# Kernel optimization log

Measured on AMD Instinct MI355X. Metric: run time of the kernel, lower is better.

## Reference

```python
import jax, jax.numpy as jnp
import numpy as np
from jax import lax
from jax.scipy.ndimage import map_coordinates

L = 10  # unrolled iterations (LayerNo)


def _conv(x, w, b):
    # x [N,C,H,W], w [O,I,3,3] -> 'SAME' padding == padding=1 for k=3
    y = lax.conv_general_dilated(x, w, (1, 1), 'SAME',
                                 dimension_numbers=('NCHW', 'OIHW', 'NCHW'))
    return y + b[None, :, None, None]


def _prelu(x, a):
    return jnp.where(x >= 0, x, a * x)


def _block(x, w1, b1, a1, w2, b2, a2, w3, b3):
    x = _prelu(_conv(x, w1, b1), a1)
    x = _prelu(_conv(x, w2, b2), a2)
    return _conv(x, w3, b3)


def _radon_forward(img, theta, det_count):
    # img [S,S]; parallel-beam line integrals -> [A, det_count]
    S = img.shape[0]
    c = (S - 1) / 2.0
    s = jnp.arange(det_count, dtype=img.dtype) - (det_count - 1) / 2.0
    t = jnp.arange(S, dtype=img.dtype) - (S - 1) / 2.0

    def one(a):
        ca, sa = jnp.cos(a), jnp.sin(a)
        x = s[:, None] * ca - t[None, :] * sa  # [D,S] sample cols
        y = s[:, None] * sa + t[None, :] * ca  # [D,S] sample rows
        vals = map_coordinates(img, [y + c, x + c], order=1, mode='constant', cval=0.0)
        return vals.sum(axis=1)

    return jax.vmap(one)(theta)


def _radon_backprojection(sino, theta, S):
    # sino [A,D] -> [S,S] (adjoint smear with bilinear detector interpolation)
    A, D = sino.shape
    c = (S - 1) / 2.0
    dc = (D - 1) / 2.0
    ax = jnp.arange(S, dtype=sino.dtype) - c
    Y, X = jnp.meshgrid(ax, ax, indexing='ij')  # row=y, col=x

    def one(row, a):
        ca, sa = jnp.cos(a), jnp.sin(a)
        sidx = (X * ca + Y * sa + dc).ravel()
        return map_coordinates(row, [sidx], order=1, mode='constant', cval=0.0).reshape(S, S)

    return jax.vmap(one)(sino, theta).sum(axis=0)


def _filter_sinogram(sino):
    # Ram-Lak ramp filter along detector axis with FBP normalization pi/(2*A)
    A, D = sino.shape
    n = 2048  # next power of two >= 2*D (D=729)
    F = jnp.fft.rfft(sino, n=n, axis=-1)
    ramp = (2.0 * jnp.fft.rfftfreq(n)).astype(sino.dtype)
    out = jnp.fft.irfft(F * ramp, n=n, axis=-1)[..., :D]
    return out * (jnp.pi / (2.0 * A))


def _forward(cond, x0, g, theta, theta_label,
             dw1, db1, da1, dw2, db2, da2, dw3, db3,
             pw1, pb1, pa1, pw2, pb2, pa2, pw3, pb3):
    S = x0.shape[2]
    A, D = g.shape[2], g.shape[3]
    h = jnp.zeros((1, 5, A, D), dtype=g.dtype)
    f = jnp.zeros((1, 5, S, S), dtype=g.dtype)
    for i in range(L):
        Op_f = _radon_forward(f[0, 1], theta, D)[None, None]          # [1,1,A,D]
        h = h + _block(jnp.concatenate([h, Op_f, g], axis=1),
                       dw1[i], db1[i], da1[i], dw2[i], db2[i], da2[i], dw3[i], db3[i])
        h1 = _filter_sinogram(h[0, 0])                                 # [A,D]
        OpAdj_h = _radon_backprojection(h1, theta, S)[None, None]      # [1,1,S,S]
        f = f + _block(jnp.concatenate([f, OpAdj_h], axis=1),
                       pw1[i], pb1[i], pa1[i], pw2[i], pb2[i], pa2[i], pw3[i], pb3[i])
    return (f[:, 0:1], f[:, 0:1], f[:, 0:1])


def setup_inputs() -> dict:
    key = jax.random.key(0)
    ks = jax.random.split(key, 12)
    S, A, D = 512, 60, 729

    def xavier(k, shp):
        cout, cin = shp[1], shp[2]
        std = np.sqrt(2.0 / ((cin + cout) * 9.0)).astype(np.float32)
        return jax.random.normal(k, shp, dtype=jnp.float32) * std

    ang = jnp.linspace(0.0, np.pi, A, endpoint=False).astype(jnp.float32)
    return {
        'cond': jax.random.normal(ks[0], (1, 1, S, S), dtype=jnp.float32),
        'x0': jax.random.normal(ks[1], (1, 1, S, S), dtype=jnp.float32),
        'g': jax.random.normal(ks[2], (1, 1, A, D), dtype=jnp.float32),
        'theta': ang,
        'theta_label': ang,
        'dw1': xavier(ks[3], (L, 32, 7, 3, 3)), 'db1': jnp.zeros((L, 32), jnp.float32), 'da1': 0.25 * jnp.ones((L,), jnp.float32),
        'dw2': xavier(ks[4], (L, 32, 32, 3, 3)), 'db2': jnp.zeros((L, 32), jnp.float32), 'da2': 0.25 * jnp.ones((L,), jnp.float32),
        'dw3': xavier(ks[5], (L, 5, 32, 3, 3)), 'db3': jnp.zeros((L, 5), jnp.float32),
        'pw1': xavier(ks[6], (L, 32, 6, 3, 3)), 'pb1': jnp.zeros((L, 32), jnp.float32), 'pa1': 0.25 * jnp.ones((L,), jnp.float32),
        'pw2': xavier(ks[7], (L, 32, 32, 3, 3)), 'pb2': jnp.zeros((L, 32), jnp.float32), 'pa2': 0.25 * jnp.ones((L,), jnp.float32),
        'pw3': xavier(ks[8], (L, 5, 32, 3, 3)), 'pb3': jnp.zeros((L, 5), jnp.float32),
    }


def reference(cond, x0, g, theta, theta_label,
              dw1, db1, da1, dw2, db2, da2, dw3, db3,
              pw1, pb1, pa1, pw2, pb2, pa2, pw3, pb3):
    return _forward(cond, x0, g, theta, theta_label,
                    dw1, db1, da1, dw2, db2, da2, dw3, db3,
                    pw1, pb1, pa1, pw2, pb2, pa2, pw3, pb3)
```

## Files before the change

### kernel.cpp

```cpp
#include <hip/hip_runtime.h>
#include <math.h>

#define SS 512
#define AANG 60
#define DDET 729
#define NPIX (SS*SS)
#define NSIN (AANG*DDET)
#define NTAPS 1457
#define DRS 768

typedef float v4u __attribute__((ext_vector_type(4), aligned(4)));
typedef float v4a __attribute__((ext_vector_type(4), aligned(16)));
typedef float v2u __attribute__((ext_vector_type(2), aligned(8)));
typedef float v2a __attribute__((ext_vector_type(2), aligned(4)));
typedef short short8 __attribute__((ext_vector_type(8)));
typedef float f32x4 __attribute__((ext_vector_type(4)));

__device__ inline unsigned short f2bf(float x){
  unsigned u = __float_as_uint(x);
  return (unsigned short)((u + 0x7fffu + ((u >> 16) & 1u)) >> 16);
}

__global__ void trig_kernel(const float* __restrict__ theta, float* __restrict__ trig){
  int a = threadIdx.x;
  if (a < AANG){ trig[a] = cosf(theta[a]); trig[AANG+a] = sinf(theta[a]); }
}

__global__ void taps_kernel(float* __restrict__ taps){
  __shared__ double red[256];
  int m  = blockIdx.x;
  int mm = m - 728;
  double s = 0.0;
  for (int k = 1 + (int)threadIdx.x; k <= 1023; k += 256){
    int phase = (k*mm) & 2047;
    s += (double)k * cos((double)phase * (M_PI/1024.0));
  }
  red[threadIdx.x] = s;
  __syncthreads();
  for (int off=128; off; off>>=1){
    if ((int)threadIdx.x < off) red[threadIdx.x] += red[threadIdx.x+off];
    __syncthreads();
  }
  if (threadIdx.x==0){
    double x = (red[0]*(1.0/512.0) + ((mm & 1) ? -1.0 : 1.0)) / 2048.0;
    taps[m] = (float)(x * (M_PI/120.0));
  }
}

__global__ void transpose_all(const float* __restrict__ s2, float* __restrict__ d2,
                              const float* __restrict__ s5, float* __restrict__ d5){
  int idx = blockIdx.x*256 + (int)threadIdx.x;
  const float* src; float* dst;
  int Cout = 5, Cin = 32;
  if      (idx < 14400){              src=s2; dst=d2; }
  else if (idx < 28800){ idx-=14400;  src=s5; dst=d5; }
  else return;
  int t = idx % 9; int r = idx/9;
  int i = r % Cin; r /= Cin;
  int o = r % Cout; int l = r/Cout;
  dst[((l*Cin+i)*9+t)*Cout+o] = src[idx];
}

__global__ void transpose_w8(const float* __restrict__ src, float* __restrict__ dst, int Cin){
  int idx = blockIdx.x*256 + (int)threadIdx.x;
  int tot = 10*32*Cin*9;
  if (idx >= tot) return;
  int t = idx % 9; int r = idx/9;
  int i = r % Cin; r /= Cin;
  int o = r % 32; int l = r/32;
  int cg = o >> 3, u = o & 7;
  dst[(((l*Cin + i)*4 + cg)*9 + t)*8 + u] = src[idx];
}

__global__ void prep_bimg(const float* __restrict__ w, unsigned short* __restrict__ B){
  int idx = blockIdx.x*256 + (int)threadIdx.x;
  if (idx >= 10*9*2*64*8) return;
  int j    =  idx        & 7;
  int lane = (idx >> 3)  & 63;
  int n    = (idx >> 9)  & 1;
  int r    =  idx >> 10;
  int tap = r % 9, l = r / 9;
  int c = (lane >> 4)*8 + j;
  int o = n*16 + (lane & 15);
  float x = w[(((size_t)(l*32+o)*32 + c)*9) + tap];
  unsigned short hb = f2bf(x);
  float hf = __uint_as_float((unsigned)hb << 16);
  unsigned short lb = f2bf(x - hf);
  size_t d = (size_t)l*18432 + (size_t)tap*2048 + n*1024 + lane*8 + j;
  B[d]       = hb;
  B[d + 512] = lb;
}

__global__ void prep_bimg3(const float* __restrict__ w, unsigned short* __restrict__ B){
  int idx = blockIdx.x*256 + (int)threadIdx.x;
  if (idx >= 10*9*64*8) return;
  int j    =  idx       & 7;
  int lane = (idx >> 3) & 63;
  int r    =  idx >> 9;
  int tap = r % 9, l = r / 9;
  int c = (lane >> 4)*8 + j;
  int o = lane & 15;
  float x = (o < 5) ? w[(((size_t)(l*5+o)*32 + c)*9) + tap] : 0.f;
  unsigned short hb = f2bf(x);
  float hf = __uint_as_float((unsigned)hb << 16);
  unsigned short lb = f2bf(x - hf);
  size_t d = (size_t)l*9216 + (size_t)tap*1024 + lane*8 + j;
  B[d]       = hb;
  B[d + 512] = lb;
}

__device__ inline void clipr(float al, float ial, float be, float lo, float hi,
                             float& A, float& B, bool& empty){
  if (fabsf(al) < 1e-7f){ if (be < lo || be > hi) empty = true; return; }
  float t0 = (lo - be)*ial, t1 = (hi - be)*ial;
  float mn = fminf(t0,t1), mx = fmaxf(t0,t1);
  A = fmaxf(A, mn); B = fminf(B, mx);
}

__device__ inline float samp_guard(const float* __restrict__ base, float aR, float bR,
                                   float aC, float bC, int t){
  float tp = (float)t - 255.5f;
  float R = fmaf(aR, tp, bR);
  float C = fmaf(aC, tp, bC);
  float rf = floorf(R), cf = floorf(C);
  int r0 = (int)rf, c0 = (int)cf;
  int r1 = r0+1,    c1 = c0+1;
  float fr = R - rf, fc = C - cf;
  bool r0ok = (r0>=0 && r0<SS), r1ok = (r1>=0 && r1<SS);
  bool c0ok = (c0>=0 && c0<SS), c1ok = (c1>=0 && c1<SS);
  float v00 = (r0ok && c0ok) ? base[r0*SS+c0] : 0.f;
  float v01 = (r0ok && c1ok) ? base[r0*SS+c1] : 0.f;
  float v10 = (r1ok && c0ok) ? base[r1*SS+c0] : 0.f;
  float v11 = (r1ok && c1ok) ? base[r1*SS+c1] : 0.f;
  return (1.f-fr)*((1.f-fc)*v00 + fc*v01) + fr*((1.f-fc)*v10 + fc*v11);
}

__global__ __launch_bounds__(256) void radon_fwd_kernel(
    const float* __restrict__ img, const float* __restrict__ imgT,
    const float* __restrict__ trig, float* __restrict__ out){
  int gid  = blockIdx.x*4 + ((int)threadIdx.x >> 6);
  int lane = (int)threadIdx.x & 63;
  if (gid >= NSIN) return;
  int a = gid / DDET;
  int d = gid - a*DDET;
  float ca = trig[a], sa = trig[AANG+a];
  float sd = (float)d - 364.0f;
  float Rc = fmaf(sd, sa, 255.5f);
  float Cc = fmaf(sd, ca, 255.5f);
  float aR = ca, bR = Rc, aC = -sa, bC = Cc;
  const float* base = img;
  if (fabsf(ca) > fabsf(sa)){
    base = imgT;
    float tmp;
    tmp=aR; aR=aC; aC=tmp;
    tmp=bR; bR=bC; bC=tmp;
  }
  float iaR = __builtin_amdgcn_rcpf(aR);
  float iaC = __builtin_amdgcn_rcpf(aC);
  float tiA = -255.5f, tiB = 255.5f;  bool iE=false;
  float teA = -255.5f, teB = 255.5f;  bool eE=false;
  clipr(aR,iaR,bR, 0.001f, 510.999f, tiA,tiB,iE);
  clipr(aC,iaC,bC, 0.001f, 510.999f, tiA,tiB,iE);
  clipr(aR,iaR,bR, -0.999f, 511.999f, teA,teB,eE);
  clipr(aC,iaC,bC, -0.999f, 511.999f, teA,teB,eE);
  float acc = 0.f;
  if (!eE && teA <= teB){
    int eA = max(0,   (int)floorf(teA+255.5f) - 1);
    int eB = min(511, (int)ceilf (teB+255.5f) + 1);
    int iA = (int)ceilf (tiA+255.5f) + 1;
    int iB = (int)floorf(tiB+255.5f) - 1;
    iA = max(iA, eA); iB = min(iB, eB);
    if (iE || iA > iB){
      for (int t = eA+lane; t <= eB; t += 64) acc += samp_guard(base,aR,bR,aC,bC,t);
    } else {
      for (int t = eA+lane;   t <  iA; t += 64) acc += samp_guard(base,aR,bR,aC,bC,t);
      for (int t = iB+1+lane; t <= eB; t += 64) acc += samp_guard(base,aR,bR,aC,bC,t);
      for (int t = iA+lane;   t <= iB; t += 64){
        float tp = (float)t - 255.5f;
        float R = fmaf(aR, tp, bR);
        float C = fmaf(aC, tp, bC);
        int r0 = (int)R, c0 = (int)C;
        float fr = R - (float)r0, fc = C - (float)c0;
        const float* p = base + r0*SS + c0;
        float v00 = p[0], v01 = p[1], v10 = p[SS], v11 = p[SS+1];
        float top = v00 + fc*(v01-v00);
        float bot = v10 + fc*(v11-v10);
        acc += top + fr*(bot-top);
      }
    }
  }
  for (int off=32; off; off>>=1) acc += __shfl_down(acc, off);
  if (lane==0) out[gid] = acc;
}

__global__ __launch_bounds__(256) void filter_kernel2(
    const float* __restrict__ h0, const float* __restrict__ taps,
    float* __restrict__ h1){
  __shared__ float red[256];
  int a  = blockIdx.x / 12;
  int jb = blockIdx.x - a*12;
  int jl = (int)threadIdx.x & 63;
  int kq = (int)threadIdx.x >> 6;
  int j  = jb*64 + jl;
  float acc = 0.f;
  if (j < DDET){
    const float* row = h0 + a*DDET;
    const float* tp  = taps + 728 + j;
    int k0 = kq*183;
    int k1 = min(k0+183, DDET);
    for (int k=k0;k<k1;k++) acc = fmaf(row[k], tp[-k], acc);
  }
  red[threadIdx.x] = acc;
  __syncthreads();
  if ((int)threadIdx.x < 64 && j < DDET){
    float s = red[jl] + red[64+jl] + red[128+jl] + red[192+jl];
    h1[a*DDET + j] = s;
  }
}

__global__ __launch_bounds__(256) void backproj_kernel(
    const float* __restrict__ h1, const float* __restrict__ trig,
    float* __restrict__ out){
  __shared__ float sh[AANG*28];
  __shared__ int   sbase[AANG];
  __shared__ float strig[2*AANG];
  int tid = threadIdx.x;
  int x0 = (blockIdx.x & 31) * 16, y0 = (blockIdx.x >> 5) * 16;
  if (tid < 2*AANG) strig[tid] = trig[tid];
  __syncthreads();
  if (tid < AANG){
    float ca = strig[tid], sa = strig[AANG+tid];
    float Xa = (float)x0 - 255.5f, Xb = Xa + 15.f;
    float Ya = (float)y0 - 255.5f, Yb = Ya + 15.f;
    float s00 = Xa*ca + Ya*sa, s01 = Xb*ca + Ya*sa;
    float s10 = Xa*ca + Yb*sa, s11 = Xb*ca + Yb*sa;
    float mn = fminf(fminf(s00,s01), fminf(s10,s11)) + 364.0f;
    sbase[tid] = (int)floorf(mn) - 2;
  }
  __syncthreads();
  for (int s = tid; s < AANG*28; s += 256){
    int a = s / 28, j = s - a*28;
    int idx = sbase[a] + j;
    sh[s] = (idx >= 0 && idx < DDET) ? h1[a*DDET + idx] : 0.f;
  }
  __syncthreads();
  int x = x0 + (tid & 15), y = y0 + (tid >> 4);
  float X = (float)x - 255.5f, Y = (float)y - 255.5f;
  float acc = 0.f;
  #pragma unroll 6
  for (int a=0;a<AANG;a++){
    float sidx = fmaf(X, strig[a], fmaf(Y, strig[AANG+a], 364.0f));
    float ff = floorf(sidx);
    int k = (int)ff - sbase[a];
    float fi = sidx - ff;
    float v0 = sh[a*28+k], v1 = sh[a*28+k+1];
    acc += v0 + fi*(v1-v0);
  }
  out[y*SS+x] = acc;
}

__global__ __launch_bounds__(256) void conv3x3_dual1(
    const float* __restrict__ in1, int Cin1,
    const float* __restrict__ in2, int Cin2,
    const float* __restrict__ wt,
    const float* __restrict__ bias, const float* __restrict__ prelu,
    unsigned short* __restrict__ outHi, unsigned short* __restrict__ outLo)
{
  const int W = DDET, HW = NSIN;
  int pix = blockIdx.x*256 + (int)threadIdx.x;
  if (pix >= NSIN) return;
  int cg = blockIdx.y;
  int y = pix / W, x = pix - y*W;
  bool ym = y>0, yp = y<AANG-1, xm = x>0, xp = x<W-1;
  float acc[8];
  #pragma unroll
  for (int o=0;o<8;o++) acc[o] = bias[cg*8+o];
  const float* wch = wt + cg*72;
  for (int part=0; part<2; part++){
    const float* src = part ? in2 : in1;
    int nch = part ? Cin2 : Cin1;
    const float* ip = src + pix;
    for (int i=0;i<nch;i++, ip+=HW, wch+=288){
      float p4 = ip[0];
      float p0=0,p1=0,p2=0,p3=0,p5=0,p6=0,p7=0,p8=0;
      if (ym){ p1 = ip[-W]; if (xm) p0 = ip[-W-1]; if (xp) p2 = ip[-W+1]; }
      if (xm) p3 = ip[-1];
      if (xp) p5 = ip[1];
      if (yp){ p7 = ip[W]; if (xm) p6 = ip[W-1]; if (xp) p8 = ip[W+1]; }
      float p[9] = {p0,p1,p2,p3,p4,p5,p6,p7,p8};
      #pragma unroll
      for (int t=0;t<9;t++){
        float v = p[t];
        #pragma unroll
        for (int o=0;o<8;o++) acc[o] = fmaf(v, wch[t*8+o], acc[o]);
      }
    }
  }
  float aa = *prelu;
  short8 vh, vl;
  #pragma unroll
  for (int o=0;o<8;o++){
    float s = acc[o];
    s = (s>=0.f) ? s : aa*s;
    unsigned short hb = f2bf(s);
    float hf = __uint_as_float((unsigned)hb << 16);
    unsigned short lb = f2bf(s - hf);
    vh[o] = (short)hb; vl[o] = (short)lb;
  }
  size_t base = ((size_t)(y+1)*DRS + x)*32 + cg*8;
  *(short8*)(outHi + base) = vh;
  *(short8*)(outLo + base) = vl;
}

__global__ __launch_bounds__(256) void dual_mfma32(
    const unsigned short* __restrict__ hiB, const unsigned short* __restrict__ loB,
    const unsigned short* __restrict__ Bimg,
    const float* __restrict__ bias, const float* __restrict__ prelu,
    float* __restrict__ out)
{
  int y  = blockIdx.y;
  int wv = (int)threadIdx.x >> 6;
  int lane = (int)threadIdx.x & 63;
  int xw = blockIdx.x*256 + wv*64;
  int lm = lane & 15, lq = lane >> 4;
  int laneoff = lm*32 + lq*8;
  f32x4 acc[4][2];
  #pragma unroll
  for (int s=0;s<4;s++){ acc[s][0] = (f32x4)0.f; acc[s][1] = (f32x4)0.f; }
  const short8* Bf = (const short8*)Bimg;
  #pragma unroll
  for (int dy=-1; dy<=1; dy++){
    const unsigned short* rh = hiB + (size_t)(y+dy+1)*DRS*32;
    const unsigned short* rl = loB + (size_t)(y+dy+1)*DRS*32;
    #pragma unroll
    for (int dx=-1; dx<=1; dx++){
      int tap = (dy+1)*3 + (dx+1);
      const short8* bp8 = Bf + tap*256 + lane;
      short8 bh0 = bp8[0];
      short8 bl0 = bp8[64];
      short8 bh1 = bp8[128];
      short8 bl1 = bp8[192];
      int xoff = (xw + dx)*32 + laneoff;
      #pragma unroll
      for (int s=0; s<4; s++){
        short8 ah = *(const short8*)(rh + xoff + s*512);
        short8 al = *(const short8*)(rl + xoff + s*512);
        acc[s][0] = __builtin_amdgcn_mfma_f32_16x16x32_bf16(ah, bh0, acc[s][0], 0,0,0);
        acc[s][1] = __builtin_amdgcn_mfma_f32_16x16x32_bf16(ah, bh1, acc[s][1], 0,0,0);
        acc[s][0] = __builtin_amdgcn_mfma_f32_16x16x32_bf16(al, bh0, acc[s][0], 0,0,0);
        acc[s][1] = __builtin_amdgcn_mfma_f32_16x16x32_bf16(al, bh1, acc[s][1], 0,0,0);
        acc[s][0] = __builtin_amdgcn_mfma_f32_16x16x32_bf16(ah, bl0, acc[s][0], 0,0,0);
        acc[s][1] = __builtin_amdgcn_mfma_f32_16x16x32_bf16(ah, bl1, acc[s][1], 0,0,0);
      }
    }
  }
  float aa = *prelu;
  #pragma unroll
  for (int s=0;s<4;s++){
    int px0 = xw + s*16 + lq*4;
    #pragma unroll
    for (int n=0;n<2;n++){
      int o = n*16 + lm;
      float bv = bias[o];
      f32x4 v = acc[s][n];
      v.x+=bv; v.y+=bv; v.z+=bv; v.w+=bv;
      v.x=(v.x>=0.f)?v.x:aa*v.x; v.y=(v.y>=0.f)?v.y:aa*v.y;
      v.z=(v.z>=0.f)?v.z:aa*v.z; v.w=(v.w>=0.f)?v.w:aa*v.w;
      float* op = out + (size_t)o*NSIN + y*DDET + px0;
      if (px0 + 3 <= DDET-1){
        v4u st; st.x=v.x; st.y=v.y; st.z=v.z; st.w=v.w;
        *(v4u*)op = st;
      } else {
        if (px0   <= DDET-1) op[0] = v.x;
        if (px0+1 <= DDET-1) op[1] = v.y;
        if (px0+2 <= DDET-1) op[2] = v.z;
      }
    }
  }
}

template<int COUT, int W>
__global__ __launch_bounds__(256) void conv3x3_fast2(
    const float* __restrict__ in1, int Cin1,
    const float* __restrict__ wt,
    const float* __restrict__ bias,
    float* __restrict__ out, int H)
{
  __shared__ float red[128*COUT];
  int HW = H*W;
  int pl = (int)threadIdx.x & 127;
  int half = (int)threadIdx.x >> 7;
  int pix = blockIdx.x*128 + pl;
  bool valid = (pix < HW);
  float acc[COUT];
  #pragma unroll
  for (int o=0;o<COUT;o++) acc[o] = 0.f;
  if (valid){
    int y = pix / W, x = pix - y*W;
    bool ym = y>0, yp = y<H-1, xm = x>0, xp = x<W-1;
    int nch = Cin1 >> 1;
    const float* wr = wt + half*nch*9*COUT;
    const float* ip = in1 + pix + (size_t)half*nch*HW;
    for (int i=0;i<nch;i++, ip+=HW){
      float p4 = ip[0];
      float p0=0,p1=0,p2=0,p3=0,p5=0,p6=0,p7=0,p8=0;
      if (ym){ p1 = ip[-W]; if (xm) p0 = ip[-W-1]; if (xp) p2 = ip[-W+1]; }
      if (xm) p3 = ip[-1];
      if (xp) p5 = ip[1];
      if (yp){ p7 = ip[W]; if (xm) p6 = ip[W-1]; if (xp) p8 = ip[W+1]; }
      float p[9] = {p0,p1,p2,p3,p4,p5,p6,p7,p8};
      #pragma unroll
      for (int t=0;t<9;t++){
        float v = p[t];
        #pragma unroll
        for (int o=0;o<COUT;o++) acc[o] = fmaf(v, wr[t*COUT+o], acc[o]);
      }
      wr += 9*COUT;
    }
  }
  if (half == 1){
    #pragma unroll
    for (int o=0;o<COUT;o++) red[pl*COUT+o] = acc[o];
  }
  __syncthreads();
  if (half == 0 && valid){
    float* op = out + pix;
    #pragma unroll
    for (int o=0;o<COUT;o++)
      op[o*HW] += acc[o] + red[pl*COUT+o] + bias[o];
  }
}

__device__ inline void loadrow6(float* R, const float* p, bool valid, bool lE, bool rE){
  if (valid){
    v4u a = *(const v4u*)(p-1);
    v2a b = *(const v2a*)(p+3);
    R[0]=lE?0.f:a.x; R[1]=a.y; R[2]=a.z; R[3]=a.w;
    R[4]=b.x; R[5]=rE?0.f:b.y;
  } else {
    #pragma unroll
    for (int k=0;k<6;k++) R[k]=0.f;
  }
}

__global__ __launch_bounds__(256) void conv3x3_quad6(
    const float* __restrict__ in,
    const float* __restrict__ wt,
    const float* __restrict__ bias, const float* __restrict__ prelu,
    unsigned short* __restrict__ outHi, unsigned short* __restrict__ outLo)
{
  const int W = SS, HW = NPIX;
  int rb = blockIdx.x;
  int cg = blockIdx.y;
  int yb = ((rb & 7) << 5) | (rb >> 3);
  int wv = (int)threadIdx.x >> 6;
  int lane = (int)threadIdx.x & 63;
  int y = yb*2 + (wv >> 1);
  int xb = ((wv & 1) << 8) + lane*4;
  const float* wch = wt + cg*72;
  float acc[4][8];
  #pragma unroll
  for (int px=0;px<4;px++)
    #pragma unroll
    for (int o=0;o<8;o++) acc[px][o] = 0.f;
  bool ym = y>0, yp = y<SS-1;
  bool lE = (xb==0), rE = (xb==508);
  const float* ip = in + y*W + xb;
  for (int i=0;i<6;i++, ip+=HW, wch+=288){
    float R[3][6];
    loadrow6(R[0], ip - W, ym,   lE, rE);
    loadrow6(R[1], ip,     true, lE, rE);
    loadrow6(R[2], ip + W, yp,   lE, rE);
    #pragma unroll
    for (int dy=0;dy<3;dy++){
      #pragma unroll
      for (int dx=0;dx<3;dx++){
        #pragma unroll
        for (int o=0;o<8;o++){
          float w = wch[(dy*3+dx)*8+o];
          #pragma unroll
          for (int px=0;px<4;px++)
            acc[px][o] = fmaf(R[dy][px+dx], w, acc[px][o]);
        }
      }
    }
  }
  float aa = *prelu;
  #pragma unroll
  for (int px=0;px<4;px++){
    short8 vh, vl;
    #pragma unroll
    for (int o=0;o<8;o++){
      float s = acc[px][o] + bias[cg*8+o];
      s = (s>=0.f) ? s : aa*s;
      unsigned short hb = f2bf(s);
      float hf = __uint_as_float((unsigned)hb << 16);
      unsigned short lb = f2bf(s - hf);
      vh[o] = (short)hb; vl[o] = (short)lb;
    }
    size_t base = ((size_t)(y*W + xb + px))*32 + cg*8;
    *(short8*)(outHi + base) = vh;
    *(short8*)(outLo + base) = vl;
  }
}

__global__ __launch_bounds__(256) void conv_mfma32(
    const unsigned short* __restrict__ hiB, const unsigned short* __restrict__ loB,
    const unsigned short* __restrict__ Bimg,
    const float* __restrict__ bias, const float* __restrict__ prelu,
    unsigned short* __restrict__ outHi, unsigned short* __restrict__ outLo)
{
  __shared__ unsigned int tr[4][64][33];
  int b = blockIdx.x;
  int by = b >> 1, half = b & 1;
  int y = ((by & 7) << 6) | (by >> 3);
  int wv = (int)threadIdx.x >> 6;
  int lane = (int)threadIdx.x & 63;
  int xw = half*256 + wv*64;
  int lm = lane & 15, lq = lane >> 4;
  int laneoff = lm*32 + lq*8;
  f32x4 acc[4][2];
  #pragma unroll
  for (int s=0;s<4;s++){ acc[s][0] = (f32x4)0.f; acc[s][1] = (f32x4)0.f; }
  bool fastx = (xw != 0) && (xw != 448);
  const short8* Bf = (const short8*)Bimg;
  #pragma unroll
  for (int dy=-1; dy<=1; dy++){
    int yy = y + dy;
    if ((unsigned)yy >= 512u) continue;
    const unsigned short* rh = hiB + (size_t)yy*512*32;
    const unsigned short* rl = loB + (size_t)yy*512*32;
    #pragma unroll
    for (int dx=-1; dx<=1; dx++){
      int tap = (dy+1)*3 + (dx+1);
      const short8* bp8 = Bf + tap*256 + lane;
      short8 bh0 = bp8[0];
      short8 bl0 = bp8[64];
      short8 bh1 = bp8[128];
      short8 bl1 = bp8[192];
      int xoff = (xw + dx)*32 + laneoff;
      #pragma unroll
      for (int s=0; s<4; s++){
        short8 ah, al;
        const unsigned short* ph = rh + xoff + s*512;
        const unsigned short* pl = rl + xoff + s*512;
        if (fastx){
          ah = *(const short8*)ph;
          al = *(const short8*)pl;
        } else {
          int x = xw + s*16 + lm + dx;
          bool ok = ((unsigned)x < 512u);
          ah = ok ? *(const short8*)ph : (short8)0;
          al = ok ? *(const short8*)pl : (short8)0;
        }
        acc[s][0] = __builtin_amdgcn_mfma_f32_16x16x32_bf16(ah, bh0, acc[s][0], 0,0,0);
        acc[s][1] = __builtin_amdgcn_mfma_f32_16x16x32_bf16(ah, bh1, acc[s][1], 0,0,0);
        acc[s][0] = __builtin_amdgcn_mfma_f32_16x16x32_bf16(al, bh0, acc[s][0], 0,0,0);
        acc[s][1] = __builtin_amdgcn_mfma_f32_16x16x32_bf16(al, bh1, acc[s][1], 0,0,0);
        acc[s][0] = __builtin_amdgcn_mfma_f32_16x16x32_bf16(ah, bl0, acc[s][0], 0,0,0);
        acc[s][1] = __builtin_amdgcn_mfma_f32_16x16x32_bf16(ah, bl1, acc[s][1], 0,0,0);
      }
    }
  }
  float aa = *prelu;
  #pragma unroll
  for (int s=0;s<4;s++){
    #pragma unroll
    for (int n=0;n<2;n++){
      int o = n*16 + lm;
      float bv = bias[o];
      f32x4 v = acc[s][n];
      v.x+=bv; v.y+=bv; v.z+=bv; v.w+=bv;
      v.x=(v.x>=0.f)?v.x:aa*v.x; v.y=(v.y>=0.f)?v.y:aa*v.y;
      v.z=(v.z>=0.f)?v.z:aa*v.z; v.w=(v.w>=0.f)?v.w:aa*v.w;
      #pragma unroll
      for (int r=0;r<4;r++){
        float x = v[r];
        unsigned short hb = f2bf(x);
        float hf = __uint_as_float((unsigned)hb << 16);
        unsigned short lb = f2bf(x - hf);
        tr[wv][s*16 + lq*4 + r][o] = ((unsigned)hb << 16) | (unsigned)lb;
      }
    }
  }
  __syncthreads();
  int c8 = lane & 3;
  int pxl = lane >> 2;
  #pragma unroll
  for (int k=0;k<4;k++){
    int px = pxl + k*16;
    short8 vh, vl;
    #pragma unroll
    for (int j=0;j<8;j++){
      unsigned p = tr[wv][px][c8*8 + j];
      vh[j] = (short)(p >> 16);
      vl[j] = (short)(p & 0xffffu);
    }
    size_t base = ((size_t)(y*SS + xw + px))*32 + c8*8;
    *(short8*)(outHi + base) = vh;
    *(short8*)(outLo + base) = vl;
  }
}

__global__ __launch_bounds__(256) void duo_mfma(
    const unsigned short* __restrict__ hiB, const unsigned short* __restrict__ loB,
    const unsigned short* __restrict__ Bimg3,
    const float* __restrict__ bias,
    float* __restrict__ f,
    float* __restrict__ fout, float* __restrict__ tout)
{
  int b = blockIdx.x;
  int by = b >> 1, half = b & 1;
  int y = ((by & 7) << 6) | (by >> 3);
  int wv = (int)threadIdx.x >> 6;
  int lane = (int)threadIdx.x & 63;
  int xw = half*256 + wv*64;
  int lm = lane & 15, lq = lane >> 4;
  int laneoff = lm*32 + lq*8;
  f32x4 acc[4];
  #pragma unroll
  for (int s=0;s<4;s++) acc[s] = (f32x4)0.f;
  bool fastx = (xw != 0) && (xw != 448);
  const short8* Bf = (const short8*)Bimg3;
  #pragma unroll
  for (int dy=-1; dy<=1; dy++){
    int yy = y + dy;
    if ((unsigned)yy >= 512u) continue;
    const unsigned short* rh = hiB + (size_t)yy*512*32;
    const unsigned short* rl = loB + (size_t)yy*512*32;
    #pragma unroll
    for (int dx=-1; dx<=1; dx++){
      int tap = (dy+1)*3 + (dx+1);
      const short8* bp8 = Bf + tap*128 + lane;
      short8 bh = bp8[0];
      short8 bl = bp8[64];
      int xoff = (xw + dx)*32 + laneoff;
      #pragma unroll
      for (int s=0; s<4; s++){
        short8 ah, al;
        const unsigned short* ph = rh + xoff + s*512;
        const unsigned short* pl = rl + xoff + s*512;
        if (fastx){
          ah = *(const short8*)ph;
          al = *(const short8*)pl;
        } else {
          int x = xw + s*16 + lm + dx;
          bool ok = ((unsigned)x < 512u);
          ah = ok ? *(const short8*)ph : (short8)0;
          al = ok ? *(const short8*)pl : (short8)0;
        }
        acc[s] = __builtin_amdgcn_mfma_f32_16x16x32_bf16(ah, bh, acc[s], 0,0,0);
        acc[s] = __builtin_amdgcn_mfma_f32_16x16x32_bf16(al, bh, acc[s], 0,0,0);
        acc[s] = __builtin_amdgcn_mfma_f32_16x16x32_bf16(ah, bl, acc[s], 0,0,0);
      }
    }
  }
  if (lm < 5){
    float bv = bias[lm];
    #pragma unroll
    for (int s=0;s<4;s++){
      int px0 = xw + s*16 + lq*4;
      float* op = f + (size_t)lm*NPIX + y*SS + px0;
      f32x4 old = *(const f32x4*)op;
      f32x4 v = acc[s];
      v.x += old.x + bv; v.y += old.y + bv;
      v.z += old.z + bv; v.w += old.w + bv;
      *(f32x4*)op = v;
      if (lm == 1){
        tout[(px0  )*SS + y] = v.x;
        tout[(px0+1)*SS + y] = v.y;
        tout[(px0+2)*SS + y] = v.z;
        tout[(px0+3)*SS + y] = v.w;
      }
      if (lm == 0 && fout){
        float* q = fout + y*SS + px0;
        *(f32x4*)q = v;
        *(f32x4*)(q + NPIX) = v;
        *(f32x4*)(q + 2*NPIX) = v;
      }
    }
  }
}

extern "C" void kernel_launch(void* const* d_in, const int* in_sizes, int n_in,
                              void* d_out, int out_size, void* d_ws, size_t ws_size,
                              hipStream_t stream){
  const float* g     = (const float*)d_in[2];
  const float* theta = (const float*)d_in[3];
  const float* dw1 = (const float*)d_in[5];
  const float* db1 = (const float*)d_in[6];
  const float* da1 = (const float*)d_in[7];
  const float* dw2 = (const float*)d_in[8];
  const float* db2 = (const float*)d_in[9];
  const float* da2 = (const float*)d_in[10];
  const float* dw3 = (const float*)d_in[11];
  const float* db3 = (const float*)d_in[12];
  const float* pw1 = (const float*)d_in[13];
  const float* pb1 = (const float*)d_in[14];
  const float* pa1 = (const float*)d_in[15];
  const float* pw2 = (const float*)d_in[16];
  const float* pb2 = (const float*)d_in[17];
  const float* pa2 = (const float*)d_in[18];
  const float* pw3 = (const float*)d_in[19];
  const float* pb3 = (const float*)d_in[20];

  float* ws     = (float*)d_ws;
  float* trig   = ws;
  float* taps   = ws + 128;
  float* h      = ws + 2048;
  float* opf    = h + 5*NSIN;
  float* gcopy  = opf + NSIN;
  float* h1     = gcopy + NSIN;
  float* f      = h1 + NSIN;
  float* bp     = f + 5*NPIX;
  float* imgT   = bp + NPIX;
  float* dualT1 = imgT + NPIX;
  float* dualT2 = dualT1 + 32*NSIN;
  float* primT2slot = dualT2 + 32*NSIN;
  unsigned short* primHi = (unsigned short*)primT2slot;
  unsigned short* primLo = primHi + (size_t)32*NPIX;
  unsigned short* nhwcHi = (unsigned short*)(primT2slot + 32*NPIX);
  unsigned short* nhwcLo = nhwcHi + (size_t)32*NPIX;
  float* wsp   = (float*)(nhwcLo + (size_t)32*NPIX);
  float* wtd3  = wsp;
  float* wtp3  = wsp + 14400;
  float* wtd1b = wsp + 28800;
  float* wtd2b = wsp + 48960;
  float* wtp1b = wsp + 141120;
  unsigned short* Bimg  = (unsigned short*)(wsp + 158400);
  unsigned short* Bimg2 = Bimg + 184320;
  unsigned short* Bimg3 = Bimg2 + 184320;
  const size_t DUALSZ = (size_t)64 + (size_t)62*DRS*32 + 64;
  unsigned short* dualHiRaw = Bimg3 + 92160;
  unsigned short* dualLoRaw = dualHiRaw + DUALSZ;
  unsigned short* dualHi = dualHiRaw + 64;
  unsigned short* dualLo = dualLoRaw + 64;

  hipMemsetAsync(h, 0, (size_t)(5*NSIN)*sizeof(float), stream);
  hipMemsetAsync(f, 0, (size_t)(7*NPIX)*sizeof(float), stream);
  hipMemsetAsync(dualHiRaw, 0, 2*DUALSZ*sizeof(unsigned short), stream);
  hipMemcpyAsync(gcopy, g, (size_t)NSIN*sizeof(float), hipMemcpyDeviceToDevice, stream);
  trig_kernel<<<1,64,0,stream>>>(theta, trig);
  taps_kernel<<<NTAPS,256,0,stream>>>(taps);
  transpose_all<<<(28800+255)/256,256,0,stream>>>(dw3,wtd3, pw3,wtp3);
  transpose_w8<<<(20160+255)/256,256,0,stream>>>(dw1, wtd1b, 7);
  transpose_w8<<<(17280+255)/256,256,0,stream>>>(pw1, wtp1b, 6);
  prep_bimg<<<(92160+255)/256,256,0,stream>>>(pw2, Bimg);
  prep_bimg<<<(92160+255)/256,256,0,stream>>>(dw2, Bimg2);
  prep_bimg3<<<(46080+255)/256,256,0,stream>>>(pw3, Bimg3);

  const int GD = (NSIN+255)/256;

  for (int i=0;i<10;i++){
    radon_fwd_kernel<<<(NSIN+3)/4,256,0,stream>>>(f + NPIX, imgT, trig, opf);
    conv3x3_dual1<<<dim3(GD,4),256,0,stream>>>(h, 5, opf, 2, wtd1b+(size_t)i*7*288,
                                               db1+(size_t)i*32, da1+i, dualHi, dualLo);
    dual_mfma32<<<dim3(3,AANG),256,0,stream>>>(dualHi, dualLo, Bimg2+(size_t)i*18432,
                                               db2+(size_t)i*32, da2+i, dualT2);
    conv3x3_fast2<5,DDET><<<(NSIN+127)/128,256,0,stream>>>(dualT2, 32, wtd3+i*1440, db3+(size_t)i*5, h, AANG);
    filter_kernel2<<<AANG*12,256,0,stream>>>(h, taps, h1);
    backproj_kernel<<<NPIX/256,256,0,stream>>>(h1, trig, bp);
    conv3x3_quad6<<<dim3(256,4),256,0,stream>>>(f, wtp1b+(size_t)i*6*288, pb1+(size_t)i*32, pa1+i, nhwcHi, nhwcLo);
    conv_mfma32<<<1024,256,0,stream>>>(nhwcHi, nhwcLo, Bimg+(size_t)i*18432, pb2+(size_t)i*32, pa2+i, primHi, primLo);
    duo_mfma<<<1024,256,0,stream>>>(primHi, primLo, Bimg3+(size_t)i*9216, pb3+(size_t)i*5, f,
                                    (i==9) ? (float*)d_out : nullptr, imgT);
  }
}
```

Before: 2.065 ms.

## Replace primal first conv with bf16x3 MFMA kernel using packed NHWC8 input

The scalar FP32 primal first-layer conv (6->32 channels) is replaced by an MFMA kernel that uses split hi/lo bf16 products. Its input is a new 8-channel interleaved hi/lo buffer: duo_mfma writes channels 0-4 of it and backproj writes channel 5, so the separate fp32 backprojection image is no longer needed. The kernel transposes its results through LDS to write NHWC output. The dual_mfma32 launch also changes to single-wave 64-thread blocks for more blocks, at the cost of extra bf16 conversion and scatter stores in producer kernels.

```diff
diff --git a/kernel.cpp b/kernel.cpp
--- a/kernel.cpp
+++ b/kernel.cpp
@@ -14,6 +14,7 @@
 typedef float v2u __attribute__((ext_vector_type(2), aligned(8)));
 typedef float v2a __attribute__((ext_vector_type(2), aligned(4)));
 typedef short short8 __attribute__((ext_vector_type(8)));
+typedef short short4v __attribute__((ext_vector_type(4)));
 typedef float f32x4 __attribute__((ext_vector_type(4)));
 
 __device__ inline unsigned short f2bf(float x){
@@ -105,6 +106,25 @@
   float hf = __uint_as_float((unsigned)hb << 16);
   unsigned short lb = f2bf(x - hf);
   size_t d = (size_t)l*9216 + (size_t)tap*1024 + lane*8 + j;
+  B[d]       = hb;
+  B[d + 512] = lb;
+}
+
+__global__ void prep_bimg1(const float* __restrict__ w, unsigned short* __restrict__ B){
+  int idx = blockIdx.x*256 + (int)threadIdx.x;
+  if (idx >= 10*3*2*64*8) return;
+  int j    =  idx       & 7;
+  int lane = (idx >> 3) & 63;
+  int n    = (idx >> 9) & 1;
+  int r    =  idx >> 10;
+  int g = r % 3, l = r / 3;
+  int t = g*4 + (lane >> 4);
+  int o = n*16 + (lane & 15);
+  float x = (t < 9 && j < 6) ? w[(((size_t)(l*32+o)*6 + j)*9) + t] : 0.f;
+  unsigned short hb = f2bf(x);
+  float hf = __uint_as_float((unsigned)hb << 16);
+  unsigned short lb = f2bf(x - hf);
+  size_t d = (size_t)l*6144 + (size_t)g*2048 + n*1024 + lane*8 + j;
   B[d]       = hb;
   B[d + 512] = lb;
 }
@@ -220,7 +240,7 @@
 
 __global__ __launch_bounds__(256) void backproj_kernel(
     const float* __restrict__ h1, const float* __restrict__ trig,
-    float* __restrict__ out){
+    unsigned short* __restrict__ hi8, unsigned short* __restrict__ lo8){
   __shared__ float sh[AANG*28];
   __shared__ int   sbase[AANG];
   __shared__ float strig[2*AANG];
@@ -256,7 +276,12 @@
     float v0 = sh[a*28+k], v1 = sh[a*28+k+1];
     acc += v0 + fi*(v1-v0);
   }
-  out[y*SS+x] = acc;
+  unsigned short hb = f2bf(acc);
+  float hf = __uint_as_float((unsigned)hb << 16);
+  unsigned short lb = f2bf(acc - hf);
+  size_t p8 = ((size_t)(y*SS + x))*8 + 5;
+  hi8[p8] = hb;
+  lo8[p8] = lb;
 }
 
 __global__ __launch_bounds__(256) void conv3x3_dual1(
@@ -312,16 +337,15 @@
   *(short8*)(outLo + base) = vl;
 }
 
-__global__ __launch_bounds__(256) void dual_mfma32(
+__global__ __launch_bounds__(64) void dual_mfma32(
     const unsigned short* __restrict__ hiB, const unsigned short* __restrict__ loB,
     const unsigned short* __restrict__ Bimg,
     const float* __restrict__ bias, const float* __restrict__ prelu,
     float* __restrict__ out)
 {
   int y  = blockIdx.y;
-  int wv = (int)threadIdx.x >> 6;
-  int lane = (int)threadIdx.x & 63;
-  int xw = blockIdx.x*256 + wv*64;
+  int lane = (int)threadIdx.x;
+  int xw = blockIdx.x*64;
   int lm = lane & 15, lq = lane >> 4;
   int laneoff = lm*32 + lq*8;
   f32x4 acc[4][2];
@@ -431,74 +455,93 @@
   }
 }
 
-__device__ inline void loadrow6(float* R, const float* p, bool valid, bool lE, bool rE){
-  if (valid){
-    v4u a = *(const v4u*)(p-1);
-    v2a b = *(const v2a*)(p+3);
-    R[0]=lE?0.f:a.x; R[1]=a.y; R[2]=a.z; R[3]=a.w;
-    R[4]=b.x; R[5]=rE?0.f:b.y;
-  } else {
-    #pragma unroll
-    for (int k=0;k<6;k++) R[k]=0.f;
-  }
-}
-
-__global__ __launch_bounds__(256) void conv3x3_quad6(
-    const float* __restrict__ in,
-    const float* __restrict__ wt,
+__global__ __launch_bounds__(256) void prim1_mfma(
+    const unsigned short* __restrict__ hi8, const unsigned short* __restrict__ lo8,
+    const unsigned short* __restrict__ Bimg1,
     const float* __restrict__ bias, const float* __restrict__ prelu,
     unsigned short* __restrict__ outHi, unsigned short* __restrict__ outLo)
 {
-  const int W = SS, HW = NPIX;
-  int rb = blockIdx.x;
-  int cg = blockIdx.y;
-  int yb = ((rb & 7) << 5) | (rb >> 3);
+  __shared__ unsigned int tr[4][64][33];
+  int b = blockIdx.x;
+  int by = b >> 1, half = b & 1;
+  int y = ((by & 7) << 6) | (by >> 3);
   int wv = (int)threadIdx.x >> 6;
   int lane = (int)threadIdx.x & 63;
-  int y = yb*2 + (wv >> 1);
-  int xb = ((wv & 1) << 8) + lane*4;
-  const float* wch = wt + cg*72;
-  float acc[4][8];
-  #pragma unroll
-  for (int px=0;px<4;px++)
-    #pragma unroll
-    for (int o=0;o<8;o++) acc[px][o] = 0.f;
-  bool ym = y>0, yp = y<SS-1;
-  bool lE = (xb==0), rE = (xb==508);
-  const float* ip = in + y*W + xb;
-  for (int i=0;i<6;i++, ip+=HW, wch+=288){
-    float R[3][6];
-    loadrow6(R[0], ip - W, ym,   lE, rE);
-    loadrow6(R[1], ip,     true, lE, rE);
-    loadrow6(R[2], ip + W, yp,   lE, rE);
-    #pragma unroll
-    for (int dy=0;dy<3;dy++){
+  int xw = half*256 + wv*64;
+  int lm = lane & 15, lq = lane >> 4;
+  f32x4 acc[4][2];
+  #pragma unroll
+  for (int s=0;s<4;s++){ acc[s][0] = (f32x4)0.f; acc[s][1] = (f32x4)0.f; }
+  bool fast = (y>0) && (y<511) && (xw!=0) && (xw!=448);
+  const short8* Bf = (const short8*)Bimg1;
+  #pragma unroll
+  for (int g=0; g<3; g++){
+    const short8* bp8 = Bf + g*256 + lane;
+    short8 bh0 = bp8[0];
+    short8 bl0 = bp8[64];
+    short8 bh1 = bp8[128];
+    short8 bl1 = bp8[192];
+    int t = g*4 + lq; if (t > 8) t = 8;
+    int dy = (t >= 6) ? 1 : ((t >= 3) ? 0 : -1);
+    int dx = t - (dy+1)*3 - 1;
+    int row = y + dy;
+    #pragma unroll
+    for (int s=0; s<4; s++){
+      short8 ah, al;
+      int px = xw + s*16 + lm + dx;
+      if (fast){
+        size_t off = ((size_t)row*SS + px)*8;
+        ah = *(const short8*)(hi8 + off);
+        al = *(const short8*)(lo8 + off);
+      } else {
+        bool ok = ((unsigned)row < 512u) && ((unsigned)px < 512u);
+        size_t off = ok ? ((size_t)row*SS + px)*8 : 0;
+        ah = ok ? *(const short8*)(hi8 + off) : (short8)0;
+        al = ok ? *(const short8*)(lo8 + off) : (short8)0;
+      }
+      acc[s][0] = __builtin_amdgcn_mfma_f32_16x16x32_bf16(ah, bh0, acc[s][0], 0,0,0);
+      acc[s][1] = __builtin_amdgcn_mfma_f32_16x16x32_bf16(ah, bh1, acc[s][1], 0,0,0);
+      acc[s][0] = __builtin_amdgcn_mfma_f32_16x16x32_bf16(al, bh0, acc[s][0], 0,0,0);
+      acc[s][1] = __builtin_amdgcn_mfma_f32_16x16x32_bf16(al, bh1, acc[s][1], 0,0,0);
+      acc[s][0] = __builtin_amdgcn_mfma_f32_16x16x32_bf16(ah, bl0, acc[s][0], 0,0,0);
+      acc[s][1] = __builtin_amdgcn_mfma_f32_16x16x32_bf16(ah, bl1, acc[s][1], 0,0,0);
+    }
+  }
+  float aa = *prelu;
+  #pragma unroll
+  for (int s=0;s<4;s++){
+    #pragma unroll
+    for (int n=0;n<2;n++){
+      int o = n*16 + lm;
+      float bv = bias[o];
+      f32x4 v = acc[s][n];
+      v.x+=bv; v.y+=bv; v.z+=bv; v.w+=bv;
+      v.x=(v.x>=0.f)?v.x:aa*v.x; v.y=(v.y>=0.f)?v.y:aa*v.y;
+      v.z=(v.z>=0.f)?v.z:aa*v.z; v.w=(v.w>=0.f)?v.w:aa*v.w;
       #pragma unroll
-      for (int dx=0;dx<3;dx++){
-        #pragma unroll
-        for (int o=0;o<8;o++){
-          float w = wch[(dy*3+dx)*8+o];
-          #pragma unroll
-          for (int px=0;px<4;px++)
-            acc[px][o] = fmaf(R[dy][px+dx], w, acc[px][o]);
-        }
-      }
-    }
-  }
-  float aa = *prelu;
-  #pragma unroll
-  for (int px=0;px<4;px++){
+      for (int r=0;r<4;r++){
+        float x = v[r];
+        unsigned short hb = f2bf(x);
+        float hf = __uint_as_float((unsigned)hb << 16);
+        unsigned short lb = f2bf(x - hf);
+        tr[wv][s*16 + lq*4 + r][o] = ((unsigned)hb << 16) | (unsigned)lb;
+      }
+    }
+  }
+  __syncthreads();
+  int c8 = lane & 3;
+  int pxl = lane >> 2;
+  #pragma unroll
+  for (int k=0;k<4;k++){
+    int px = pxl + k*16;
     short8 vh, vl;
     #pragma unroll
-    for (int o=0;o<8;o++){
-      float s = acc[px][o] + bias[cg*8+o];
-      s = (s>=0.f) ? s : aa*s;
-      unsigned short hb = f2bf(s);
-      float hf = __uint_as_float((unsigned)hb << 16);
-      unsigned short lb = f2bf(s - hf);
-      vh[o] = (short)hb; vl[o] = (short)lb;
-    }
-    size_t base = ((size_t)(y*W + xb + px))*32 + cg*8;
+    for (int j=0;j<8;j++){
+      unsigned p = tr[wv][px][c8*8 + j];
+      vh[j] = (short)(p >> 16);
+      vl[j] = (short)(p & 0xffffu);
+    }
+    size_t base = ((size_t)(y*SS + xw + px))*32 + c8*8;
     *(short8*)(outHi + base) = vh;
     *(short8*)(outLo + base) = vl;
   }
@@ -607,8 +650,10 @@
     const unsigned short* __restrict__ Bimg3,
     const float* __restrict__ bias,
     float* __restrict__ f,
-    float* __restrict__ fout, float* __restrict__ tout)
+    float* __restrict__ fout, float* __restrict__ tout,
+    unsigned short* __restrict__ hi8, unsigned short* __restrict__ lo8)
 {
+  __shared__ unsigned int t8[4][64][6];
   int b = blockIdx.x;
   int by = b >> 1, half = b & 1;
   int y = ((by & 7) << 6) | (by >> 3);
@@ -666,6 +711,14 @@
       v.x += old.x + bv; v.y += old.y + bv;
       v.z += old.z + bv; v.w += old.w + bv;
       *(f32x4*)op = v;
+      #pragma unroll
+      for (int r=0;r<4;r++){
+        float x = v[r];
+        unsigned short hb = f2bf(x);
+        float hf = __uint_as_float((unsigned)hb << 16);
+        unsigned short lb = f2bf(x - hf);
+        t8[wv][s*16 + lq*4 + r][lm] = ((unsigned)hb << 16) | (unsigned)lb;
+      }
       if (lm == 1){
         tout[(px0  )*SS + y] = v.x;
         tout[(px0+1)*SS + y] = v.y;
@@ -679,6 +732,18 @@
         *(f32x4*)(q + 2*NPIX) = v;
       }
     }
+  }
+  __syncthreads();
+  {
+    unsigned c0 = t8[wv][lane][0], c1 = t8[wv][lane][1], c2 = t8[wv][lane][2];
+    unsigned c3 = t8[wv][lane][3], c4 = t8[wv][lane][4];
+    size_t base = ((size_t)(y*SS + xw + lane))*8;
+    short4v vh; vh[0]=(short)(c0>>16); vh[1]=(short)(c1>>16); vh[2]=(short)(c2>>16); vh[3]=(short)(c3>>16);
+    short4v vl; vl[0]=(short)(c0&0xffffu); vl[1]=(short)(c1&0xffffu); vl[2]=(short)(c2&0xffffu); vl[3]=(short)(c3&0xffffu);
+    *(short4v*)(hi8 + base) = vh;
+    *(short4v*)(lo8 + base) = vl;
+    hi8[base+4] = (unsigned short)(c4>>16);
+    lo8[base+4] = (unsigned short)(c4&0xffffu);
   }
 }
 
@@ -730,24 +795,28 @@
   unsigned short* Bimg  = (unsigned short*)(wsp + 158400);
   unsigned short* Bimg2 = Bimg + 184320;
   unsigned short* Bimg3 = Bimg2 + 184320;
+  unsigned short* Bimg1 = Bimg3 + 92160;
   const size_t DUALSZ = (size_t)64 + (size_t)62*DRS*32 + 64;
-  unsigned short* dualHiRaw = Bimg3 + 92160;
+  unsigned short* dualHiRaw = Bimg1 + 61440;
   unsigned short* dualLoRaw = dualHiRaw + DUALSZ;
   unsigned short* dualHi = dualHiRaw + 64;
   unsigned short* dualLo = dualLoRaw + 64;
+  unsigned short* nh8Hi = dualLoRaw + DUALSZ;
+  unsigned short* nh8Lo = nh8Hi + (size_t)NPIX*8;
 
   hipMemsetAsync(h, 0, (size_t)(5*NSIN)*sizeof(float), stream);
   hipMemsetAsync(f, 0, (size_t)(7*NPIX)*sizeof(float), stream);
   hipMemsetAsync(dualHiRaw, 0, 2*DUALSZ*sizeof(unsigned short), stream);
+  hipMemsetAsync(nh8Hi, 0, (size_t)2*NPIX*8*sizeof(unsigned short), stream);
   hipMemcpyAsync(gcopy, g, (size_t)NSIN*sizeof(float), hipMemcpyDeviceToDevice, stream);
   trig_kernel<<<1,64,0,stream>>>(theta, trig);
   taps_kernel<<<NTAPS,256,0,stream>>>(taps);
   transpose_all<<<(28800+255)/256,256,0,stream>>>(dw3,wtd3, pw3,wtp3);
   transpose_w8<<<(20160+255)/256,256,0,stream>>>(dw1, wtd1b, 7);
-  transpose_w8<<<(17280+255)/256,256,0,stream>>>(pw1, wtp1b, 6);
   prep_bimg<<<(92160+255)/256,256,0,stream>>>(pw2, Bimg);
   prep_bimg<<<(92160+255)/256,256,0,stream>>>(dw2, Bimg2);
   prep_bimg3<<<(46080+255)/256,256,0,stream>>>(pw3, Bimg3);
+  prep_bimg1<<<(30720+255)/256,256,0,stream>>>(pw1, Bimg1);
 
   const int GD = (NSIN+255)/256;
 
@@ -755,14 +824,15 @@
     radon_fwd_kernel<<<(NSIN+3)/4,256,0,stream>>>(f + NPIX, imgT, trig, opf);
     conv3x3_dual1<<<dim3(GD,4),256,0,stream>>>(h, 5, opf, 2, wtd1b+(size_t)i*7*288,
                                                db1+(size_t)i*32, da1+i, dualHi, dualLo);
-    dual_mfma32<<<dim3(3,AANG),256,0,stream>>>(dualHi, dualLo, Bimg2+(size_t)i*18432,
+    dual_mfma32<<<dim3(12,AANG),64,0,stream>>>(dualHi, dualLo, Bimg2+(size_t)i*18432,
                                                db2+(size_t)i*32, da2+i, dualT2);
     conv3x3_fast2<5,DDET><<<(NSIN+127)/128,256,0,stream>>>(dualT2, 32, wtd3+i*1440, db3+(size_t)i*5, h, AANG);
     filter_kernel2<<<AANG*12,256,0,stream>>>(h, taps, h1);
-    backproj_kernel<<<NPIX/256,256,0,stream>>>(h1, trig, bp);
-    conv3x3_quad6<<<dim3(256,4),256,0,stream>>>(f, wtp1b+(size_t)i*6*288, pb1+(size_t)i*32, pa1+i, nhwcHi, nhwcLo);
+    backproj_kernel<<<NPIX/256,256,0,stream>>>(h1, trig, nh8Hi, nh8Lo);
+    prim1_mfma<<<1024,256,0,stream>>>(nh8Hi, nh8Lo, Bimg1+(size_t)i*6144,
+                                      pb1+(size_t)i*32, pa1+i, nhwcHi, nhwcLo);
     conv_mfma32<<<1024,256,0,stream>>>(nhwcHi, nhwcLo, Bimg+(size_t)i*18432, pb2+(size_t)i*32, pa2+i, primHi, primLo);
     duo_mfma<<<1024,256,0,stream>>>(primHi, primLo, Bimg3+(size_t)i*9216, pb3+(size_t)i*5, f,
-                                    (i==9) ? (float*)d_out : nullptr, imgT);
-  }
-}
+                                    (i==9) ? (float*)d_out : nullptr, imgT, nh8Hi, nh8Lo);
+  }
+}
```

New measurement: 1.882 ms. -8.9%, faster.
